# Performance work log

Measured on AMD Instinct MI355X. Metric: run time of the kernel, lower is better.

The kernel has to match this reference:

```python
import jax, jax.numpy as jnp
import numpy as np

B, S, T, H, NH, NL = 16, 128, 64, 128, 8, 4
DH = H // NH
FF = 2 * H
SCALE = 1.0 / float(np.sqrt(DH))


def _ln(x, s, b):
    m = x.mean(-1, keepdims=True)
    v = ((x - m) ** 2).mean(-1, keepdims=True)
    return (x - m) * jax.lax.rsqrt(v + 1e-5) * s + b


def _block(x, mask, p):
    Wq, bq, Wk, bk, Wv, bv, Wo, bo, s1, c1, W1, d1, W2, d2, s2, c2 = p
    N, L, _ = x.shape
    q = (x @ Wq + bq).reshape(N, L, NH, DH)
    k = (x @ Wk + bk).reshape(N, L, NH, DH)
    v = (x @ Wv + bv).reshape(N, L, NH, DH)
    scores = jnp.einsum('nqhd,nkhd->nhqk', q, k) * SCALE
    scores = jnp.where(mask[:, None, :, :], scores, -1e9)
    a = jax.nn.softmax(scores, axis=-1)
    o = jnp.einsum('nhqk,nkhd->nqhd', a, v).reshape(N, L, H)
    x = _ln(x + o @ Wo + bo, s1, c1)
    h = jax.nn.relu(x @ W1 + d1)
    return _ln(x + h @ W2 + d2, s2, c2)


def setup_inputs():
    key = jax.random.key(0)
    ks = jax.random.split(key, 16)
    g = lambda k, shape: jax.random.normal(k, shape, jnp.float32) * 0.02
    return {
        'polylines': jax.random.normal(ks[0], (B, S, T, H), jnp.float32),
        'lengths': jax.random.randint(ks[1], (B, S), 0, T + 1),
        'proj_w': g(ks[2], (H, H)), 'proj_b': jnp.zeros((H,), jnp.float32),
        'proj_ln_s': jnp.ones((H,), jnp.float32), 'proj_ln_b': jnp.zeros((H,), jnp.float32),
        'pos_emb': g(ks[3], (1, T, H)),
        'Wq': g(ks[4], (NL, H, H)), 'bq': jnp.zeros((NL, H), jnp.float32),
        'Wk': g(ks[5], (NL, H, H)), 'bk': jnp.zeros((NL, H), jnp.float32),
        'Wv': g(ks[6], (NL, H, H)), 'bv': jnp.zeros((NL, H), jnp.float32),
        'Wo': g(ks[7], (NL, H, H)), 'bo': jnp.zeros((NL, H), jnp.float32),
        'ln1_s': jnp.ones((NL, H), jnp.float32), 'ln1_b': jnp.zeros((NL, H), jnp.float32),
        'W1': g(ks[8], (NL, H, FF)), 'b1': jnp.zeros((NL, FF), jnp.float32),
        'W2': g(ks[9], (NL, FF, H)), 'b2': jnp.zeros((NL, H), jnp.float32),
        'ln2_s': jnp.ones((NL, H), jnp.float32), 'ln2_b': jnp.zeros((NL, H), jnp.float32),
    }


def reference(polylines, lengths, proj_w, proj_b, proj_ln_s, proj_ln_b, pos_emb,
              Wq, bq, Wk, bk, Wv, bv, Wo, bo, ln1_s, ln1_b, W1, b1, W2, b2, ln2_s, ln2_b):
    # valid[b,s,t] = t < lengths[b,s]; lengths==0 -> polyline absent (fully padded)
    valid = jnp.arange(T)[None, None, :] < lengths[:, :, None]  # [B,S,T]
    x = jnp.where(valid[..., None], polylines, -1.0)            # -1 pad as in np.pad(constant_values=-1)
    # mask_temporal[b,s] = outer(valid[b,s], valid[b,s])
    mask_t = (valid[:, :, :, None] & valid[:, :, None, :]).reshape(B * S, T, T)
    # mask_spatial[b,t] = outer(valid[b,:,t], valid[b,:,t])
    vs = jnp.transpose(valid, (0, 2, 1))                        # [B,T,S]
    mask_s = (vs[:, :, :, None] & vs[:, :, None, :]).reshape(B * T, S, S)

    x = x.reshape(B * S, T, H)
    x = jax.nn.relu(_ln(x @ proj_w + proj_b, proj_ln_s, proj_ln_b))  # MLP: Linear->LN->ReLU
    x = x + pos_emb[:, :T, :]

    mask = mask_t
    for i in range(NL):
        if i == NL // 2:
            # switch from temporal to spatial attention: [B*S,T,H] -> [B*T,S,H]
            x = x.reshape(B, S, T, H).transpose(0, 2, 1, 3).reshape(B * T, S, H)
            mask = mask_s
        p = (Wq[i], bq[i], Wk[i], bk[i], Wv[i], bv[i], Wo[i], bo[i],
             ln1_s[i], ln1_b[i], W1[i], b1[i], W2[i], b2[i], ln2_s[i], ln2_b[i])
        x = _block(x, mask, p)
    # faithful to original final reshape (treats [B*T,S,H] buffer as [B,S,T,H])
    return x.reshape(B, S, T, H)[:, 0, :]
```

## Files before the change

kernel.cpp:

```cpp
#include <hip/hip_runtime.h>

typedef short short8 __attribute__((ext_vector_type(8)));
typedef short short4_t __attribute__((ext_vector_type(4)));
typedef float floatx4 __attribute__((ext_vector_type(4)));
typedef unsigned short ushort_t;

#define B_ 16
#define S_ 128
#define T_ 64
#define H_ 128
#define FF_ 256
#define SCALEQK 0.25f

#define OFFP 0
#define OFFQ(l) (16384 + (l) * 65536)
#define OFFK(l) (OFFQ(l) + 16384)
#define OFFV(l) (OFFQ(l) + 32768)
#define OFFO(l) (OFFQ(l) + 49152)
#define OFFW1(l) (278528 + (l) * 65536)
#define OFFW2(l) (OFFW1(l) + 32768)

__device__ __forceinline__ float b2f(ushort_t u) {
    union { unsigned int i; float f; } x; x.i = ((unsigned int)u) << 16; return x.f;
}
__device__ __forceinline__ ushort_t f2b(float f) {
    union { float f; unsigned int i; } x; x.f = f;
    unsigned int r = x.i + 0x7fffu + ((x.i >> 16) & 1u);
    return (ushort_t)(r >> 16);
}
__device__ __forceinline__ int pack2b(float a, float b) {
    return (int)f2b(a) | ((int)f2b(b) << 16);
}

struct WtEnt { const float* src; int N; int K; int nclog2; int dstoff; };
struct WtArgs { WtEnt e[25]; };

__global__ __launch_bounds__(256) void wt_kernel(WtArgs a, ushort_t* __restrict__ dst) {
    WtEnt ent = a.e[blockIdx.x];
    const int tiles_c = ent.N >> 5;
    const int nt = (ent.K >> 5) * tiles_c;
    const int t = blockIdx.y;
    if (t >= nt) return;
    const int tc = t & (tiles_c - 1);
    const int tr = t >> ent.nclog2;
    __shared__ float ld[32 * 33];
    const int tid = threadIdx.x;
#pragma unroll
    for (int i = 0; i < 4; ++i) {
        int e = tid + i * 256;
        int rr = e >> 5, cc = e & 31;
        ld[rr * 33 + cc] = ent.src[(tr * 32 + rr) * ent.N + tc * 32 + cc];
    }
    __syncthreads();
    ushort_t* d = dst + ent.dstoff;
#pragma unroll
    for (int i = 0; i < 4; ++i) {
        int e = tid + i * 256;
        int rr = e >> 5, cc = e & 31;
        d[(tc * 32 + rr) * ent.K + tr * 32 + cc] = f2b(ld[cc * 33 + rr]);
    }
}

template<int RT, int CT, int KK>
__device__ __forceinline__ void mm_g(const ushort_t* aL, int sa,
                                     const ushort_t* __restrict__ wT,
                                     int colbase, int lane, floatx4 (&acc)[RT][CT]) {
    const int l15 = lane & 15, lq8 = (lane >> 4) * 8;
#pragma unroll
    for (int r = 0; r < RT; ++r)
#pragma unroll
        for (int c = 0; c < CT; ++c) acc[r][c] = (floatx4){0.f, 0.f, 0.f, 0.f};
#pragma unroll
    for (int k0 = 0; k0 < KK; k0 += 32) {
        short8 b[CT];
#pragma unroll
        for (int c = 0; c < CT; ++c)
            b[c] = *(const short8*)&wT[(colbase + c * 16 + l15) * KK + k0 + lq8];
#pragma unroll
        for (int r = 0; r < RT; ++r) {
            short8 a = *(const short8*)&aL[(r * 16 + l15) * sa + k0 + lq8];
#pragma unroll
            for (int c = 0; c < CT; ++c)
                acc[r][c] = __builtin_amdgcn_mfma_f32_16x16x32_bf16(a, b[c], acc[r][c], 0, 0, 0);
        }
    }
}

template<int RT, int CT>
__device__ __forceinline__ void add_bias(floatx4 (&acc)[RT][CT], const float* b,
                                         int colbase, int l15) {
#pragma unroll
    for (int c = 0; c < CT; ++c) {
        float bc = b[colbase + c * 16 + l15];
#pragma unroll
        for (int r = 0; r < RT; ++r)
#pragma unroll
            for (int g = 0; g < 4; ++g) acc[r][c][g] += bc;
    }
}

template<int RT, int CT>
__device__ __forceinline__ void add_resid_reg(floatx4 (&acc)[RT][CT],
                                              const float (&res)[RT][CT][4]) {
#pragma unroll
    for (int r = 0; r < RT; ++r)
#pragma unroll
        for (int c = 0; c < CT; ++c)
#pragma unroll
            for (int g = 0; g < 4; ++g) acc[r][c][g] += res[r][c][g];
}
template<int RT, int CT>
__device__ __forceinline__ void save_resid(float (&res)[RT][CT][4],
                                           const floatx4 (&acc)[RT][CT]) {
#pragma unroll
    for (int r = 0; r < RT; ++r)
#pragma unroll
        for (int c = 0; c < CT; ++c)
#pragma unroll
            for (int g = 0; g < 4; ++g) res[r][c][g] = acc[r][c][g];
}

template<int RT, int CT>
__device__ __forceinline__ void st_n(const floatx4 (&acc)[RT][CT], ushort_t* dst, int stride,
                                     int colbase, int l15, int lq) {
#pragma unroll
    for (int r = 0; r < RT; ++r)
#pragma unroll
        for (int g = 0; g < 4; ++g) {
            int row = r * 16 + lq * 4 + g;
#pragma unroll
            for (int c = 0; c < CT; ++c)
                dst[row * stride + colbase + c * 16 + l15] = f2b(acc[r][c][g]);
        }
}

template<int RT, int CT>
__device__ __forceinline__ void st_t(const floatx4 (&acc)[RT][CT], ushort_t* dst, int stride,
                                     int colbase, int l15, int lq) {
#pragma unroll
    for (int r = 0; r < RT; ++r)
#pragma unroll
        for (int c = 0; c < CT; ++c) {
            int d = colbase + c * 16 + l15;
            short4_t p;
#pragma unroll
            for (int g = 0; g < 4; ++g) p[g] = (short)f2b(acc[r][c][g]);
            *(short4_t*)&dst[d * stride + r * 16 + lq * 4] = p;
        }
}

template<int RT, int CT>
__device__ __forceinline__ void ln_norm(floatx4 (&acc)[RT][CT], float* redL,
                                        const float* lns, const float* lnb,
                                        int colbase, int l15, int lq, int wv) {
#pragma unroll
    for (int r = 0; r < RT; ++r)
#pragma unroll
        for (int g = 0; g < 4; ++g) {
            float s = 0.f, q = 0.f;
#pragma unroll
            for (int c = 0; c < CT; ++c) { float v = acc[r][c][g]; s += v; q += v * v; }
            s += __shfl_xor(s, 1); s += __shfl_xor(s, 2); s += __shfl_xor(s, 4); s += __shfl_xor(s, 8);
            q += __shfl_xor(q, 1); q += __shfl_xor(q, 2); q += __shfl_xor(q, 4); q += __shfl_xor(q, 8);
            if (l15 == 0) {
                int row = r * 16 + lq * 4 + g;
                redL[row * 8 + wv] = s;
                redL[row * 8 + 4 + wv] = q;
            }
        }
    __syncthreads();
#pragma unroll
    for (int r = 0; r < RT; ++r)
#pragma unroll
        for (int g = 0; g < 4; ++g) {
            int row = r * 16 + lq * 4 + g;
            float4 S = *(float4*)&redL[row * 8];
            float4 Q = *(float4*)&redL[row * 8 + 4];
            float mean = (S.x + S.y + S.z + S.w) * (1.f / 128.f);
            float var = (Q.x + Q.y + Q.z + Q.w) * (1.f / 128.f) - mean * mean;
            float rstd = rsqrtf(var + 1e-5f);
#pragma unroll
            for (int c = 0; c < CT; ++c) {
                int col = colbase + c * 16 + l15;
                acc[r][c][g] = (acc[r][c][g] - mean) * rstd * lns[col] + lnb[col];
            }
        }
}

template<int JT>
__device__ __forceinline__ void softmax_pack(floatx4 (&st)[JT], bool iv, unsigned jm,
                                             int (&px)[JT][2]) {
    float ev[JT][4];
    float mx = -3.0e38f;
#pragma unroll
    for (int jt = 0; jt < JT; ++jt)
#pragma unroll
        for (int g = 0; g < 4; ++g) {
            bool ok = iv && ((jm >> (jt * 4 + g)) & 1u);
            float s = ok ? st[jt][g] * SCALEQK : -1e9f;
            ev[jt][g] = s; mx = fmaxf(mx, s);
        }
    mx = fmaxf(mx, __shfl_xor(mx, 16)); mx = fmaxf(mx, __shfl_xor(mx, 32));
    float sum = 0.f;
#pragma unroll
    for (int jt = 0; jt < JT; ++jt)
#pragma unroll
        for (int g = 0; g < 4; ++g) { float e = __expf(ev[jt][g] - mx); ev[jt][g] = e; sum += e; }
    sum += __shfl_xor(sum, 16); sum += __shfl_xor(sum, 32);
    float inv = 1.f / sum;
#pragma unroll
    for (int jt = 0; jt < JT; ++jt) {
        px[jt][0] = pack2b(ev[jt][0] * inv, ev[jt][1] * inv);
        px[jt][1] = pack2b(ev[jt][2] * inv, ev[jt][3] * inv);
    }
}

__device__ __forceinline__ short8 pfrag(const int (*px)[2], int jc, int lq, int l15) {
    const int jA = (lq & 1) * 32 + l15;
    int a0 = __shfl(px[jc * 2][0], jA);
    int a1 = __shfl(px[jc * 2][1], jA);
    int a2 = __shfl(px[jc * 2][0], jA + 16);
    int a3 = __shfl(px[jc * 2][1], jA + 16);
    int b0 = __shfl(px[jc * 2 + 1][0], jA);
    int b1 = __shfl(px[jc * 2 + 1][1], jA);
    int b2 = __shfl(px[jc * 2 + 1][0], jA + 16);
    int b3 = __shfl(px[jc * 2 + 1][1], jA + 16);
    const bool t = (lq >> 1) != 0;
    union { int4 i; short8 s; } u;
    u.i = make_int4(t ? b0 : a0, t ? b1 : a1, t ? b2 : a2, t ? b3 : a3);
    return u.s;
}
__device__ __forceinline__ short8 vfrag(const ushort_t* vT, int stride, int row, int off) {
    int2 a = *(const int2*)&vT[row * stride + off];
    int2 b = *(const int2*)&vT[row * stride + off + 4];
    union { int4 i; short8 s; } u;
    u.i = make_int4(a.x, a.y, b.x, b.y);
    return u.s;
}

__global__ __launch_bounds__(256, 2) void k1_mega(
    const float* __restrict__ poly, const int* __restrict__ lens,
    const ushort_t* __restrict__ wt,
    const float* __restrict__ projb, const float* __restrict__ pls,
    const float* __restrict__ plb, const float* __restrict__ pos,
    const float* __restrict__ bq0, const float* __restrict__ bk0,
    const float* __restrict__ bv0, const float* __restrict__ bo0,
    const float* __restrict__ l1s0, const float* __restrict__ l1b0,
    const float* __restrict__ b10, const float* __restrict__ b20,
    const float* __restrict__ l2s0, const float* __restrict__ l2b0,
    const float* __restrict__ bq1, const float* __restrict__ bk1,
    const float* __restrict__ bv1,
    ushort_t* __restrict__ o1, float* __restrict__ xr0f)
{
    __shared__ ushort_t pool[34816];
    __shared__ float redL[512];
    __shared__ float psL[8 * 68];
    __shared__ float q1L[128];
    ushort_t* xL = pool;
    ushort_t* qL = pool + 8704;
    ushort_t* kL = pool + 17408;
    ushort_t* vT = pool + 26112;
    ushort_t* hL = pool + 17408;

    const int tid = threadIdx.x, lane = tid & 63, wv = tid >> 6;
    const int l15 = lane & 15, lq = lane >> 4;
    const int gid = blockIdx.x;
    const int len = lens[gid];

    {
        const float* pg = poly + (size_t)gid * 8192;
#pragma unroll
        for (int it = 0; it < 8; ++it) {
            int e4 = (tid + it * 256) * 4;
            int row = e4 >> 7, col = e4 & 127;
            float4 f = *(const float4*)(pg + e4);
            if (row >= len) { f.x = -1.f; f.y = -1.f; f.z = -1.f; f.w = -1.f; }
            short4_t u;
            u[0] = (short)f2b(f.x); u[1] = (short)f2b(f.y);
            u[2] = (short)f2b(f.z); u[3] = (short)f2b(f.w);
            *(short4_t*)&xL[row * 136 + col] = u;
        }
    }
    __syncthreads();

    floatx4 a2[4][2];
    float xre[4][2][4];

    mm_g<4, 2, 128>(xL, 136, wt + OFFP, wv * 32, lane, a2);
    add_bias<4, 2>(a2, projb, wv * 32, l15);
    ln_norm<4, 2>(a2, redL, pls, plb, wv * 32, l15, lq, wv);
    __syncthreads();
#pragma unroll
    for (int r = 0; r < 4; ++r)
#pragma unroll
        for (int gg = 0; gg < 4; ++gg) {
            int row = r * 16 + lq * 4 + gg;
#pragma unroll
            for (int c = 0; c < 2; ++c) {
                int col = wv * 32 + c * 16 + l15;
                float v = fmaxf(a2[r][c][gg], 0.f) + pos[row * 128 + col];
                xre[r][c][gg] = v;
                xL[row * 136 + col] = f2b(v);
            }
        }
    __syncthreads();

    mm_g<4, 2, 128>(xL, 136, wt + OFFQ(0), wv * 32, lane, a2);
    add_bias<4, 2>(a2, bq0, wv * 32, l15);
    st_n<4, 2>(a2, qL, 136, wv * 32, l15, lq);
    mm_g<4, 2, 128>(xL, 136, wt + OFFK(0), wv * 32, lane, a2);
    add_bias<4, 2>(a2, bk0, wv * 32, l15);
    st_n<4, 2>(a2, kL, 136, wv * 32, l15, lq);
    mm_g<4, 2, 128>(xL, 136, wt + OFFV(0), wv * 32, lane, a2);
    add_bias<4, 2>(a2, bv0, wv * 32, l15);
    st_t<4, 2>(a2, vT, 68, wv * 32, l15, lq);
    __syncthreads();

    {
        const int iRow = wv * 16 + l15;
        const bool iv = iRow < len;
        unsigned jm = 0;
#pragma unroll
        for (int jt = 0; jt < 4; ++jt)
#pragma unroll
            for (int gg = 0; gg < 4; ++gg)
                if (jt * 16 + lq * 4 + gg < len) jm |= (1u << (jt * 4 + gg));
        for (int h = 0; h < 8; ++h) {
            const int hc = h * 16;
            short8 z8 = {0, 0, 0, 0, 0, 0, 0, 0};
            short8 bqf = z8;
            if (lq < 2) bqf = *(const short8*)&qL[iRow * 136 + hc + lq * 8];
            floatx4 st[4];
#pragma unroll
            for (int jt = 0; jt < 4; ++jt) {
                short8 ak = z8;
                if (lq < 2) ak = *(const short8*)&kL[(jt * 16 + l15) * 136 + hc + lq * 8];
                floatx4 zz = {0.f, 0.f, 0.f, 0.f};
                st[jt] = __builtin_amdgcn_mfma_f32_16x16x32_bf16(ak, bqf, zz, 0, 0, 0);
            }
            int px[4][2];
            softmax_pack<4>(st, iv, jm, px);
            floatx4 ao = {0.f, 0.f, 0.f, 0.f};
#pragma unroll
            for (int jc = 0; jc < 2; ++jc) {
                short8 av = vfrag(vT, 68, hc + l15, jc * 32 + lq * 8);
                short8 bp = pfrag(px, jc, lq, l15);
                ao = __builtin_amdgcn_mfma_f32_16x16x32_bf16(av, bp, ao, 0, 0, 0);
            }
            short4_t w;
#pragma unroll
            for (int gg = 0; gg < 4; ++gg) w[gg] = (short)f2b(ao[gg]);
            *(short4_t*)&qL[iRow * 136 + hc + lq * 4] = w;
        }
    }
    __syncthreads();

    mm_g<4, 2, 128>(qL, 136, wt + OFFO(0), wv * 32, lane, a2);
    add_bias<4, 2>(a2, bo0, wv * 32, l15);
    add_resid_reg<4, 2>(a2, xre);
    ln_norm<4, 2>(a2, redL, l1s0, l1b0, wv * 32, l15, lq, wv);
    save_resid<4, 2>(xre, a2);
    st_n<4, 2>(a2, xL, 136, wv * 32, l15, lq);
    __syncthreads();

    {
        floatx4 a4[4][4];
        mm_g<4, 4, 128>(xL, 136, wt + OFFW1(0), wv * 64, lane, a4);
        add_bias<4, 4>(a4, b10, wv * 64, l15);
#pragma unroll
        for (int r = 0; r < 4; ++r)
#pragma unroll
            for (int c = 0; c < 4; ++c)
#pragma unroll
                for (int gg = 0; gg < 4; ++gg) a4[r][c][gg] = fmaxf(a4[r][c][gg], 0.f);
        st_n<4, 4>(a4, hL, 272, wv * 64, l15, lq);
    }
    __syncthreads();

    mm_g<4, 2, 256>(hL, 272, wt + OFFW2(0), wv * 32, lane, a2);
    add_bias<4, 2>(a2, b20, wv * 32, l15);
    add_resid_reg<4, 2>(a2, xre);
    ln_norm<4, 2>(a2, redL, l2s0, l2b0, wv * 32, l15, lq, wv);
    save_resid<4, 2>(xre, a2);
    st_n<4, 2>(a2, xL, 136, wv * 32, l15, lq);
    if (lq == 0) {
#pragma unroll
        for (int c = 0; c < 2; ++c)
            xr0f[(size_t)gid * 128 + wv * 32 + c * 16 + l15] = a2[0][c][0];
    }
    __syncthreads();

    mm_g<4, 2, 128>(xL, 136, wt + OFFK(1), wv * 32, lane, a2);
    add_bias<4, 2>(a2, bk1, wv * 32, l15);
    st_n<4, 2>(a2, kL, 136, wv * 32, l15, lq);
    mm_g<4, 2, 128>(xL, 136, wt + OFFV(1), wv * 32, lane, a2);
    add_bias<4, 2>(a2, bv1, wv * 32, l15);
    st_t<4, 2>(a2, vT, 68, wv * 32, l15, lq);
    if (tid < 128) {
        int d = tid;
        float a = bq1[d];
        const ushort_t* wq = wt + OFFQ(1) + d * 128;
#pragma unroll 4
        for (int j0 = 0; j0 < 128; j0 += 8) {
            short8 w8 = *(const short8*)&wq[j0];
            short8 x8 = *(const short8*)&xL[j0];
#pragma unroll
            for (int q = 0; q < 8; ++q)
                a = fmaf(b2f((ushort_t)x8[q]), b2f((ushort_t)w8[q]), a);
        }
        q1L[d] = a;
    }
    __syncthreads();

    {
        int h = tid >> 5, jj = tid & 31;
        int hc = h * 16;
        float s[2];
#pragma unroll
        for (int half = 0; half < 2; ++half) {
            int j = jj + half * 32;
            float a = 0.f;
            short8 k0v = *(const short8*)&kL[j * 136 + hc];
            short8 k1v = *(const short8*)&kL[j * 136 + hc + 8];
#pragma unroll
            for (int q = 0; q < 8; ++q) {
                a = fmaf(q1L[hc + q], b2f((ushort_t)k0v[q]), a);
                a = fmaf(q1L[hc + 8 + q], b2f((ushort_t)k1v[q]), a);
            }
            s[half] = (j < len) ? a * SCALEQK : -1e9f;
        }
        float mx = fmaxf(s[0], s[1]);
#pragma unroll
        for (int d = 1; d < 32; d <<= 1) mx = fmaxf(mx, __shfl_xor(mx, d));
        float e0 = __expf(s[0] - mx), e1 = __expf(s[1] - mx);
        float sum = e0 + e1;
#pragma unroll
        for (int d = 1; d < 32; d <<= 1) sum += __shfl_xor(sum, d);
        float inv = 1.f / sum;
        psL[h * 68 + jj] = e0 * inv;
        psL[h * 68 + jj + 32] = e1 * inv;
    }
    __syncthreads();
    if (tid < 128) {
        int h = tid >> 4, d = tid & 15, hc = h * 16;
        float a = 0.f;
#pragma unroll 4
        for (int j0 = 0; j0 < 64; j0 += 4) {
            float4 p4 = *(const float4*)&psL[h * 68 + j0];
            short4_t v4 = *(const short4_t*)&vT[(hc + d) * 68 + j0];
            a += p4.x * b2f((ushort_t)v4[0]) + p4.y * b2f((ushort_t)v4[1])
               + p4.z * b2f((ushort_t)v4[2]) + p4.w * b2f((ushort_t)v4[3]);
        }
        o1[(size_t)gid * 128 + hc + d] = f2b(a);
    }
}

__device__ __forceinline__ void k2a_body(char* smem, int blk,
    const ushort_t* __restrict__ xg, const int* __restrict__ lens,
    const ushort_t* __restrict__ wt, int l,
    const float* __restrict__ bq, const float* __restrict__ bk,
    const float* __restrict__ bv,
    ushort_t* __restrict__ aob)
{
    ushort_t* xL = (ushort_t*)(smem);
    ushort_t* qL = (ushort_t*)(smem + 34816);
    ushort_t* kL = (ushort_t*)(smem + 40960);
    ushort_t* vT = (ushort_t*)(smem + 47104);
    int* vldL = (int*)(smem + 51456);

    const int tid = threadIdx.x, lane = tid & 63, wv = tid >> 6;
    const int l15 = lane & 15, lq = lane >> 4;
    const int g = blk >> 3, h = blk & 7, hc = h * 16;
    const size_t rowg = (size_t)g * 128;

#pragma unroll
    for (int it = 0; it < 8; ++it) {
        int e8 = tid + it * 256;
        int row = e8 >> 4, kg = e8 & 15;
        *(short8*)&xL[row * 136 + kg * 8] = *(const short8*)&xg[(rowg + row) * 128 + kg * 8];
    }
    if (tid < 128) vldL[tid] = (lens[g * 128 + tid] > 0) ? 1 : 0;
    __syncthreads();

    unsigned jm = 0;
#pragma unroll
    for (int jt = 0; jt < 8; ++jt)
#pragma unroll
        for (int gg = 0; gg < 4; ++gg)
            if (vldL[jt * 16 + lq * 4 + gg]) jm |= (1u << (jt * 4 + gg));

    {
        floatx4 a1[2][1];
        mm_g<2, 1, 128>(xL + (wv * 32) * 136, 136, wt + OFFQ(l), hc, lane, a1);
        add_bias<2, 1>(a1, bq, hc, l15);
        st_n<2, 1>(a1, qL + (wv * 32) * 24, 24, 0, l15, lq);
        mm_g<2, 1, 128>(xL + (wv * 32) * 136, 136, wt + OFFK(l), hc, lane, a1);
        add_bias<2, 1>(a1, bk, hc, l15);
        st_n<2, 1>(a1, kL + (wv * 32) * 24, 24, 0, l15, lq);
        mm_g<2, 1, 128>(xL + (wv * 32) * 136, 136, wt + OFFV(l), hc, lane, a1);
        add_bias<2, 1>(a1, bv, hc, l15);
        st_t<2, 1>(a1, vT + wv * 32, 136, 0, l15, lq);
    }
    __syncthreads();

    for (int u = 0; u < 2; ++u) {
        const int iRow = wv * 32 + u * 16 + l15;
        const bool iv = vldL[iRow] != 0;
        short8 z8 = {0, 0, 0, 0, 0, 0, 0, 0};
        short8 bqf = z8;
        if (lq < 2) bqf = *(const short8*)&qL[iRow * 24 + lq * 8];
        floatx4 st[8];
#pragma unroll
        for (int jt = 0; jt < 8; ++jt) {
            short8 ak = z8;
            if (lq < 2) ak = *(const short8*)&kL[(jt * 16 + l15) * 24 + lq * 8];
            floatx4 zz = {0.f, 0.f, 0.f, 0.f};
            st[jt] = __builtin_amdgcn_mfma_f32_16x16x32_bf16(ak, bqf, zz, 0, 0, 0);
        }
        int px[8][2];
        softmax_pack<8>(st, iv, jm, px);
        floatx4 ao = {0.f, 0.f, 0.f, 0.f};
#pragma unroll
        for (int jc = 0; jc < 4; ++jc) {
            short8 av = vfrag(vT, 136, l15, jc * 32 + lq * 8);
            short8 bp = pfrag(px, jc, lq, l15);
            ao = __builtin_amdgcn_mfma_f32_16x16x32_bf16(av, bp, ao, 0, 0, 0);
        }
        short4_t w;
#pragma unroll
        for (int gg = 0; gg < 4; ++gg) w[gg] = (short)f2b(ao[gg]);
        *(short4_t*)&aob[(rowg + iRow) * 128 + hc + lq * 4] = w;
    }
}

template<bool FINAL>
__device__ __forceinline__ void k2b_body(char* smem, int blk,
    const ushort_t* __restrict__ ain, float* __restrict__ xr,
    const ushort_t* __restrict__ wt, int l,
    const float* bo_l, const float* l1s_l, const float* l1b_l,
    const float* b1_l, const float* b2_l, const float* l2s_l, const float* l2b_l,
    ushort_t* __restrict__ xg, float* __restrict__ outp)
{
    ushort_t* aL = (ushort_t*)(smem);
    ushort_t* hL = (ushort_t*)(smem + 4352);
    float* redL = (float*)(smem + 13056);

    const int tid = threadIdx.x, lane = tid & 63, wv = tid >> 6;
    const int l15 = lane & 15, lq = lane >> 4;
    const size_t rowbase = FINAL ? ((size_t)(blk >> 2) * 128 + (blk & 3) * 16)
                                 : ((size_t)blk * 16);

    {
        int row = tid >> 4, kg = tid & 15;
        *(short8*)&aL[row * 136 + kg * 8] = *(const short8*)&ain[(rowbase + row) * 128 + kg * 8];
    }
    __syncthreads();

    floatx4 a2[1][2];
    float xre[1][2][4];

    mm_g<1, 2, 128>(aL, 136, wt + OFFO(l), wv * 32, lane, a2);
    add_bias<1, 2>(a2, bo_l, wv * 32, l15);
#pragma unroll
    for (int c = 0; c < 2; ++c)
#pragma unroll
        for (int gg = 0; gg < 4; ++gg)
            a2[0][c][gg] += xr[(rowbase + lq * 4 + gg) * 128 + wv * 32 + c * 16 + l15];
    ln_norm<1, 2>(a2, redL, l1s_l, l1b_l, wv * 32, l15, lq, wv);
    save_resid<1, 2>(xre, a2);
    st_n<1, 2>(a2, aL, 136, wv * 32, l15, lq);
    __syncthreads();

    {
        floatx4 a4[1][4];
        mm_g<1, 4, 128>(aL, 136, wt + OFFW1(l), wv * 64, lane, a4);
        add_bias<1, 4>(a4, b1_l, wv * 64, l15);
#pragma unroll
        for (int c = 0; c < 4; ++c)
#pragma unroll
            for (int gg = 0; gg < 4; ++gg) a4[0][c][gg] = fmaxf(a4[0][c][gg], 0.f);
        st_n<1, 4>(a4, hL, 272, wv * 64, l15, lq);
    }
    __syncthreads();

    mm_g<1, 2, 256>(hL, 272, wt + OFFW2(l), wv * 32, lane, a2);
    add_bias<1, 2>(a2, b2_l, wv * 32, l15);
    add_resid_reg<1, 2>(a2, xre);
    ln_norm<1, 2>(a2, redL, l2s_l, l2b_l, wv * 32, l15, lq, wv);

    if (FINAL) {
#pragma unroll
        for (int c = 0; c < 2; ++c)
#pragma unroll
            for (int gg = 0; gg < 4; ++gg) {
                int orow = (blk >> 2) * 64 + (blk & 3) * 16 + lq * 4 + gg;
                outp[(size_t)orow * 128 + wv * 32 + c * 16 + l15] = a2[0][c][gg];
            }
    } else {
#pragma unroll
        for (int c = 0; c < 2; ++c)
#pragma unroll
            for (int gg = 0; gg < 4; ++gg) {
                size_t grow = rowbase + lq * 4 + gg;
                int col = wv * 32 + c * 16 + l15;
                float v = a2[0][c][gg];
                xg[grow * 128 + col] = f2b(v);
                xr[grow * 128 + col] = v;
            }
    }
}

__device__ __forceinline__ void sync_group(unsigned* pf, int idx, unsigned target, int tid) {
    __syncthreads();
    if (tid == 0) {
        __threadfence();
        __hip_atomic_fetch_add(&pf[idx * 16], 1u, __ATOMIC_RELEASE,
                               __HIP_MEMORY_SCOPE_AGENT);
        while (__hip_atomic_load(&pf[idx * 16], __ATOMIC_ACQUIRE,
                                 __HIP_MEMORY_SCOPE_AGENT) < target)
            __builtin_amdgcn_s_sleep(8);
        __threadfence();
    }
    __syncthreads();
}

__global__ __launch_bounds__(256) void k3_tail(
    const ushort_t* __restrict__ o1buf, float* __restrict__ xrf,
    const int* __restrict__ lens, const ushort_t* __restrict__ wt,
    const float* __restrict__ bq, const float* __restrict__ bk,
    const float* __restrict__ bv, const float* __restrict__ bo,
    const float* __restrict__ l1s, const float* __restrict__ l1b,
    const float* __restrict__ b1, const float* __restrict__ b2,
    const float* __restrict__ l2s, const float* __restrict__ l2b,
    ushort_t* __restrict__ xg, ushort_t* __restrict__ aob,
    float* __restrict__ outp, unsigned* __restrict__ pf)
{
    __shared__ __align__(16) char smem[51968];
    const int t = (int)blockIdx.x;
    const int g = t >> 3, sub = t & 7;
    const int tid = threadIdx.x;

    k2b_body<false>(smem, t, o1buf, xrf, wt, 1,
                    bo + H_, l1s + H_, l1b + H_, b1 + FF_, b2 + H_, l2s + H_, l2b + H_,
                    xg, nullptr);
    sync_group(pf, g * 4 + 0, 8, tid);

    k2a_body(smem, t, xg, lens, wt, 2, bq + 2 * H_, bk + 2 * H_, bv + 2 * H_, aob);
    sync_group(pf, g * 4 + 1, 8, tid);

    k2b_body<false>(smem, t, aob, xrf, wt, 2,
                    bo + 2 * H_, l1s + 2 * H_, l1b + 2 * H_, b1 + 2 * FF_, b2 + 2 * H_,
                    l2s + 2 * H_, l2b + 2 * H_,
                    xg, nullptr);
    sync_group(pf, g * 4 + 2, 8, tid);

    k2a_body(smem, t, xg, lens, wt, 3, bq + 3 * H_, bk + 3 * H_, bv + 3 * H_, aob);
    sync_group(pf, g * 4 + 3, 8, tid);

    if (sub < 4)
        k2b_body<true>(smem, g * 4 + sub, aob, xrf, wt, 3,
                       bo + 3 * H_, l1s + 3 * H_, l1b + 3 * H_, b1 + 3 * FF_, b2 + 3 * H_,
                       l2s + 3 * H_, l2b + 3 * H_,
                       nullptr, outp);
}

extern "C" void kernel_launch(void* const* d_in, const int* in_sizes, int n_in,
                              void* d_out, int out_size, void* d_ws, size_t ws_size,
                              hipStream_t stream)
{
    const float* poly   = (const float*)d_in[0];
    const int*   lens   = (const int*)d_in[1];
    const float* proj_w = (const float*)d_in[2];
    const float* proj_b = (const float*)d_in[3];
    const float* pls    = (const float*)d_in[4];
    const float* plb    = (const float*)d_in[5];
    const float* pos    = (const float*)d_in[6];
    const float* Wq = (const float*)d_in[7];
    const float* bq = (const float*)d_in[8];
    const float* Wk = (const float*)d_in[9];
    const float* bk = (const float*)d_in[10];
    const float* Wv = (const float*)d_in[11];
    const float* bv = (const float*)d_in[12];
    const float* Wo = (const float*)d_in[13];
    const float* bo = (const float*)d_in[14];
    const float* l1s = (const float*)d_in[15];
    const float* l1b = (const float*)d_in[16];
    const float* W1 = (const float*)d_in[17];
    const float* b1 = (const float*)d_in[18];
    const float* W2 = (const float*)d_in[19];
    const float* b2 = (const float*)d_in[20];
    const float* l2s = (const float*)d_in[21];
    const float* l2b = (const float*)d_in[22];
    float* outp = (float*)d_out;

    char* base = (char*)d_ws;
    ushort_t* wt    = (ushort_t*)base;
    ushort_t* o1buf = (ushort_t*)(base + 1081344);
    float* xrf      = (float*)(base + 1605632);
    ushort_t* xgbuf = (ushort_t*)(base + 2654208);
    ushort_t* aob   = (ushort_t*)(base + 3178496);
    unsigned* pf    = (unsigned*)(base + 3702784);

    hipMemsetAsync(pf, 0, 64 * 64, stream);

    const int HH = H_ * H_, HF = H_ * FF_;
    WtArgs wa;
    wa.e[0] = {proj_w, 128, 128, 2, OFFP};
    for (int l = 0; l < 4; ++l) {
        wa.e[1 + l * 4 + 0] = {Wq + l * HH, 128, 128, 2, OFFQ(l)};
        wa.e[1 + l * 4 + 1] = {Wk + l * HH, 128, 128, 2, OFFK(l)};
        wa.e[1 + l * 4 + 2] = {Wv + l * HH, 128, 128, 2, OFFV(l)};
        wa.e[1 + l * 4 + 3] = {Wo + l * HH, 128, 128, 2, OFFO(l)};
    }
    for (int l = 0; l < 4; ++l) {
        wa.e[17 + l * 2 + 0] = {W1 + l * HF, 256, 128, 3, OFFW1(l)};
        wa.e[17 + l * 2 + 1] = {W2 + l * HF, 128, 256, 2, OFFW2(l)};
    }
    wt_kernel<<<dim3(25, 32), 256, 0, stream>>>(wa, wt);

    k1_mega<<<dim3(2048), 256, 0, stream>>>(
        poly, lens, wt,
        proj_b, pls, plb, pos,
        bq, bk, bv, bo, l1s, l1b, b1, b2, l2s, l2b,
        bq + H_, bk + H_, bv + H_,
        o1buf, xrf);

    k3_tail<<<dim3(128), 256, 0, stream>>>(
        o1buf, xrf, lens, wt,
        bq, bk, bv, bo, l1s, l1b, b1, b2, l2s, l2b,
        xgbuf, aob, outp, pf);
}
```

Measured before the change: 391.7 us.

## Split k1_mega work across 8 waves with a 2x4 row/column tile grid

The first fused kernel now launches 512 threads per block instead of 256. Each wave owns a 32-row by 32-column tile instead of all 64 rows, so the per-thread accumulator footprint is halved. The layer-norm reduction gains a row offset, and attention assigns one head per wave looping over row tiles. This aims for more waves in flight to hide latency, but it relies on the LDS pool fitting enough blocks per CU, and the 4-blocks launch bound may cause register spills.

```diff
diff --git a/kernel.cpp b/kernel.cpp
--- a/kernel.cpp
+++ b/kernel.cpp
@@ -174,6 +174,44 @@
 #pragma unroll
         for (int g = 0; g < 4; ++g) {
             int row = r * 16 + lq * 4 + g;
+            float4 S = *(float4*)&redL[row * 8];
+            float4 Q = *(float4*)&redL[row * 8 + 4];
+            float mean = (S.x + S.y + S.z + S.w) * (1.f / 128.f);
+            float var = (Q.x + Q.y + Q.z + Q.w) * (1.f / 128.f) - mean * mean;
+            float rstd = rsqrtf(var + 1e-5f);
+#pragma unroll
+            for (int c = 0; c < CT; ++c) {
+                int col = colbase + c * 16 + l15;
+                acc[r][c][g] = (acc[r][c][g] - mean) * rstd * lns[col] + lnb[col];
+            }
+        }
+}
+
+template<int RT, int CT>
+__device__ __forceinline__ void ln_normW(floatx4 (&acc)[RT][CT], float* redL,
+                                         const float* lns, const float* lnb,
+                                         int colbase, int rowbase, int l15, int lq, int wc) {
+#pragma unroll
+    for (int r = 0; r < RT; ++r)
+#pragma unroll
+        for (int g = 0; g < 4; ++g) {
+            float s = 0.f, q = 0.f;
+#pragma unroll
+            for (int c = 0; c < CT; ++c) { float v = acc[r][c][g]; s += v; q += v * v; }
+            s += __shfl_xor(s, 1); s += __shfl_xor(s, 2); s += __shfl_xor(s, 4); s += __shfl_xor(s, 8);
+            q += __shfl_xor(q, 1); q += __shfl_xor(q, 2); q += __shfl_xor(q, 4); q += __shfl_xor(q, 8);
+            if (l15 == 0) {
+                int row = rowbase + r * 16 + lq * 4 + g;
+                redL[row * 8 + wc] = s;
+                redL[row * 8 + 4 + wc] = q;
+            }
+        }
+    __syncthreads();
+#pragma unroll
+    for (int r = 0; r < RT; ++r)
+#pragma unroll
+        for (int g = 0; g < 4; ++g) {
+            int row = rowbase + r * 16 + lq * 4 + g;
             float4 S = *(float4*)&redL[row * 8];
             float4 Q = *(float4*)&redL[row * 8 + 4];
             float mean = (S.x + S.y + S.z + S.w) * (1.f / 128.f);
@@ -238,7 +276,7 @@
     return u.s;
 }
 
-__global__ __launch_bounds__(256, 2) void k1_mega(
+__global__ __launch_bounds__(512, 4) void k1_mega(
     const float* __restrict__ poly, const int* __restrict__ lens,
     const ushort_t* __restrict__ wt,
     const float* __restrict__ projb, const float* __restrict__ pls,
@@ -264,14 +302,16 @@
 
     const int tid = threadIdx.x, lane = tid & 63, wv = tid >> 6;
     const int l15 = lane & 15, lq = lane >> 4;
+    const int wc = wv & 3, wr = wv >> 2;
+    const int cb = wc * 32, rb = wr * 32;
     const int gid = blockIdx.x;
     const int len = lens[gid];
 
     {
         const float* pg = poly + (size_t)gid * 8192;
 #pragma unroll
-        for (int it = 0; it < 8; ++it) {
-            int e4 = (tid + it * 256) * 4;
+        for (int it = 0; it < 4; ++it) {
+            int e4 = (tid + it * 512) * 4;
             int row = e4 >> 7, col = e4 & 127;
             float4 f = *(const float4*)(pg + e4);
             if (row >= len) { f.x = -1.f; f.y = -1.f; f.z = -1.f; f.w = -1.f; }
@@ -283,21 +323,21 @@
     }
     __syncthreads();
 
-    floatx4 a2[4][2];
-    float xre[4][2][4];
-
-    mm_g<4, 2, 128>(xL, 136, wt + OFFP, wv * 32, lane, a2);
-    add_bias<4, 2>(a2, projb, wv * 32, l15);
-    ln_norm<4, 2>(a2, redL, pls, plb, wv * 32, l15, lq, wv);
-    __syncthreads();
-#pragma unroll
-    for (int r = 0; r < 4; ++r)
+    floatx4 a2[2][2];
+    float xre[2][2][4];
+
+    mm_g<2, 2, 128>(xL + rb * 136, 136, wt + OFFP, cb, lane, a2);
+    add_bias<2, 2>(a2, projb, cb, l15);
+    ln_normW<2, 2>(a2, redL, pls, plb, cb, rb, l15, lq, wc);
+    __syncthreads();
+#pragma unroll
+    for (int r = 0; r < 2; ++r)
 #pragma unroll
         for (int gg = 0; gg < 4; ++gg) {
-            int row = r * 16 + lq * 4 + gg;
+            int row = rb + r * 16 + lq * 4 + gg;
 #pragma unroll
             for (int c = 0; c < 2; ++c) {
-                int col = wv * 32 + c * 16 + l15;
+                int col = cb + c * 16 + l15;
                 float v = fmaxf(a2[r][c][gg], 0.f) + pos[row * 128 + col];
                 xre[r][c][gg] = v;
                 xL[row * 136 + col] = f2b(v);
@@ -305,28 +345,28 @@
         }
     __syncthreads();
 
-    mm_g<4, 2, 128>(xL, 136, wt + OFFQ(0), wv * 32, lane, a2);
-    add_bias<4, 2>(a2, bq0, wv * 32, l15);
-    st_n<4, 2>(a2, qL, 136, wv * 32, l15, lq);
-    mm_g<4, 2, 128>(xL, 136, wt + OFFK(0), wv * 32, lane, a2);
-    add_bias<4, 2>(a2, bk0, wv * 32, l15);
-    st_n<4, 2>(a2, kL, 136, wv * 32, l15, lq);
-    mm_g<4, 2, 128>(xL, 136, wt + OFFV(0), wv * 32, lane, a2);
-    add_bias<4, 2>(a2, bv0, wv * 32, l15);
-    st_t<4, 2>(a2, vT, 68, wv * 32, l15, lq);
+    mm_g<2, 2, 128>(xL + rb * 136, 136, wt + OFFQ(0), cb, lane, a2);
+    add_bias<2, 2>(a2, bq0, cb, l15);
+    st_n<2, 2>(a2, qL + rb * 136, 136, cb, l15, lq);
+    mm_g<2, 2, 128>(xL + rb * 136, 136, wt + OFFK(0), cb, lane, a2);
+    add_bias<2, 2>(a2, bk0, cb, l15);
+    st_n<2, 2>(a2, kL + rb * 136, 136, cb, l15, lq);
+    mm_g<2, 2, 128>(xL + rb * 136, 136, wt + OFFV(0), cb, lane, a2);
+    add_bias<2, 2>(a2, bv0, cb, l15);
+    st_t<2, 2>(a2, vT + rb, 68, cb, l15, lq);
     __syncthreads();
 
     {
-        const int iRow = wv * 16 + l15;
-        const bool iv = iRow < len;
+        const int h = wv, hc = h * 16;
         unsigned jm = 0;
 #pragma unroll
         for (int jt = 0; jt < 4; ++jt)
 #pragma unroll
             for (int gg = 0; gg < 4; ++gg)
                 if (jt * 16 + lq * 4 + gg < len) jm |= (1u << (jt * 4 + gg));
-        for (int h = 0; h < 8; ++h) {
-            const int hc = h * 16;
+        for (int u = 0; u < 4; ++u) {
+            const int iRow = u * 16 + l15;
+            const bool iv = iRow < len;
             short8 z8 = {0, 0, 0, 0, 0, 0, 0, 0};
             short8 bqf = z8;
             if (lq < 2) bqf = *(const short8*)&qL[iRow * 136 + hc + lq * 8];
@@ -355,47 +395,47 @@
     }
     __syncthreads();
 
-    mm_g<4, 2, 128>(qL, 136, wt + OFFO(0), wv * 32, lane, a2);
-    add_bias<4, 2>(a2, bo0, wv * 32, l15);
-    add_resid_reg<4, 2>(a2, xre);
-    ln_norm<4, 2>(a2, redL, l1s0, l1b0, wv * 32, l15, lq, wv);
-    save_resid<4, 2>(xre, a2);
-    st_n<4, 2>(a2, xL, 136, wv * 32, l15, lq);
+    mm_g<2, 2, 128>(qL + rb * 136, 136, wt + OFFO(0), cb, lane, a2);
+    add_bias<2, 2>(a2, bo0, cb, l15);
+    add_resid_reg<2, 2>(a2, xre);
+    ln_normW<2, 2>(a2, redL, l1s0, l1b0, cb, rb, l15, lq, wc);
+    save_resid<2, 2>(xre, a2);
+    st_n<2, 2>(a2, xL + rb * 136, 136, cb, l15, lq);
     __syncthreads();
 
     {
-        floatx4 a4[4][4];
-        mm_g<4, 4, 128>(xL, 136, wt + OFFW1(0), wv * 64, lane, a4);
-        add_bias<4, 4>(a4, b10, wv * 64, l15);
-#pragma unroll
-        for (int r = 0; r < 4; ++r)
+        floatx4 a4[2][4];
+        mm_g<2, 4, 128>(xL + rb * 136, 136, wt + OFFW1(0), wc * 64, lane, a4);
+        add_bias<2, 4>(a4, b10, wc * 64, l15);
+#pragma unroll
+        for (int r = 0; r < 2; ++r)
 #pragma unroll
             for (int c = 0; c < 4; ++c)
 #pragma unroll
                 for (int gg = 0; gg < 4; ++gg) a4[r][c][gg] = fmaxf(a4[r][c][gg], 0.f);
-        st_n<4, 4>(a4, hL, 272, wv * 64, l15, lq);
-    }
-    __syncthreads();
-
-    mm_g<4, 2, 256>(hL, 272, wt + OFFW2(0), wv * 32, lane, a2);
-    add_bias<4, 2>(a2, b20, wv * 32, l15);
-    add_resid_reg<4, 2>(a2, xre);
-    ln_norm<4, 2>(a2, redL, l2s0, l2b0, wv * 32, l15, lq, wv);
-    save_resid<4, 2>(xre, a2);
-    st_n<4, 2>(a2, xL, 136, wv * 32, l15, lq);
-    if (lq == 0) {
+        st_n<2, 4>(a4, hL + rb * 272, 272, wc * 64, l15, lq);
+    }
+    __syncthreads();
+
+    mm_g<2, 2, 256>(hL + rb * 272, 272, wt + OFFW2(0), cb, lane, a2);
+    add_bias<2, 2>(a2, b20, cb, l15);
+    add_resid_reg<2, 2>(a2, xre);
+    ln_normW<2, 2>(a2, redL, l2s0, l2b0, cb, rb, l15, lq, wc);
+    save_resid<2, 2>(xre, a2);
+    st_n<2, 2>(a2, xL + rb * 136, 136, cb, l15, lq);
+    if (wr == 0 && lq == 0) {
 #pragma unroll
         for (int c = 0; c < 2; ++c)
-            xr0f[(size_t)gid * 128 + wv * 32 + c * 16 + l15] = a2[0][c][0];
-    }
-    __syncthreads();
-
-    mm_g<4, 2, 128>(xL, 136, wt + OFFK(1), wv * 32, lane, a2);
-    add_bias<4, 2>(a2, bk1, wv * 32, l15);
-    st_n<4, 2>(a2, kL, 136, wv * 32, l15, lq);
-    mm_g<4, 2, 128>(xL, 136, wt + OFFV(1), wv * 32, lane, a2);
-    add_bias<4, 2>(a2, bv1, wv * 32, l15);
-    st_t<4, 2>(a2, vT, 68, wv * 32, l15, lq);
+            xr0f[(size_t)gid * 128 + cb + c * 16 + l15] = a2[0][c][0];
+    }
+    __syncthreads();
+
+    mm_g<2, 2, 128>(xL + rb * 136, 136, wt + OFFK(1), cb, lane, a2);
+    add_bias<2, 2>(a2, bk1, cb, l15);
+    st_n<2, 2>(a2, kL + rb * 136, 136, cb, l15, lq);
+    mm_g<2, 2, 128>(xL + rb * 136, 136, wt + OFFV(1), cb, lane, a2);
+    add_bias<2, 2>(a2, bv1, cb, l15);
+    st_t<2, 2>(a2, vT + rb, 68, cb, l15, lq);
     if (tid < 128) {
         int d = tid;
         float a = bq1[d];
@@ -412,7 +452,7 @@
     }
     __syncthreads();
 
-    {
+    if (tid < 256) {
         int h = tid >> 5, jj = tid & 31;
         int hc = h * 16;
         float s[2];
@@ -718,7 +758,7 @@
     }
     wt_kernel<<<dim3(25, 32), 256, 0, stream>>>(wa, wt);
 
-    k1_mega<<<dim3(2048), 256, 0, stream>>>(
+    k1_mega<<<dim3(2048), 512, 0, stream>>>(
         poly, lens, wt,
         proj_b, pls, plb, pos,
         bq, bk, bv, bo, l1s, l1b, b1, b2, l2s, l2b,
```

Measured after the change: 430.0 us. +9.8%, slower.
